# Kernel optimization log

Measured on AMD Instinct MI355X. Metric: run time of the kernel, lower is better.

The kernel has to match this reference:

```python
import jax, jax.numpy as jnp
import numpy as np

N, D = 8192, 256
NEG_BIG = -9e15


def setup_inputs() -> dict:
    key = jax.random.key(0)
    k1, k2, k3 = jax.random.split(key, 3)
    h = jax.random.normal(k1, (N, D), dtype=jnp.float32)
    adj = jax.random.randint(k2, (N, N), 0, 2, dtype=jnp.int32)
    # xavier_uniform for a of shape (2D, 1): bound = sqrt(6/(2D+1))
    bound = np.sqrt(6.0 / (2 * D + 1)).astype(np.float32)
    a = jax.random.uniform(k3, (2 * D, 1), dtype=jnp.float32, minval=-bound, maxval=bound)
    return {"h": h, "adj": adj, "a": a}


def reference(h, adj, a):
    d = h.shape[1]
    h1 = h @ a[:d]            # [N, 1]
    h2 = h @ a[d:]            # [N, 1]
    e = jax.nn.leaky_relu(h1 + h2.T, negative_slope=0.01)  # [N, N]
    attention = jnp.where(adj > 0, e, NEG_BIG)
    attention = jax.nn.softmax(attention, axis=1)
    # dropout skipped: eval mode (training=False)
    return attention @ h      # [N, D]
```

## Files before the change

kernel.cpp:

```cpp
#include <hip/hip_runtime.h>
#include <hip/hip_bf16.h>

#define NTOT 8192
#define DDIM 256
#define ROWS 32
#define JCHUNK (NTOT / 8)
#define NITER (JCHUNK / 32)
#define NWORDS (NTOT / 32)
#define NTSTR 131584

typedef __attribute__((ext_vector_type(8))) short short8;
typedef __attribute__((ext_vector_type(4))) float floatx4;

__global__ __launch_bounds__(256) void gat_scores(const float* __restrict__ h,
                                                  const float* __restrict__ a,
                                                  float* __restrict__ s1,
                                                  float* __restrict__ s2,
                                                  float4* __restrict__ rc,
                                                  float2* __restrict__ etab) {
  int row  = blockIdx.x * 4 + (threadIdx.x >> 6);
  int lane = threadIdx.x & 63;
  const float* hr = h + (size_t)row * DDIM;
  float p1 = 0.f, p2 = 0.f;
#pragma unroll
  for (int k = 0; k < DDIM / 64; ++k) {
    int idx  = lane + 64 * k;
    float hv = hr[idx];
    p1 += hv * a[idx];
    p2 += hv * a[DDIM + idx];
  }
#pragma unroll
  for (int off = 32; off > 0; off >>= 1) {
    p1 += __shfl_down(p1, off, 64);
    p2 += __shfl_down(p2, off, 64);
  }
  if (lane == 0) {
    s1[row] = p1; s2[row] = p2;
    rc[row]   = make_float4(__expf(p1), __expf(0.01f * p1), __expf(-p1), 0.f);
    etab[row] = make_float2(__expf(p2), __expf(0.01f * p2));
  }
}

__global__ __launch_bounds__(256) void gat_pack(const int* __restrict__ adj,
                                                unsigned* __restrict__ bitsT) {
  __shared__ unsigned words[64][65];
  const int t    = threadIdx.x;
  const int lane = t & 63;
  const int w    = t >> 6;
  const int r0   = blockIdx.x * 64;
  const int jb   = blockIdx.y * 2048;

#pragma unroll 2
  for (int rr = 0; rr < 16; ++rr) {
    const int rl = w * 16 + rr;
    const int* ap = adj + (size_t)(r0 + rl) * NTOT + jb + lane * 4;
#pragma unroll
    for (int R = 0; R < 8; ++R) {
      int4 v = *(const int4*)(ap + R * 256);
      unsigned nib = (v.x > 0 ? 1u : 0u) | (v.y > 0 ? 2u : 0u) |
                     (v.z > 0 ? 4u : 0u) | (v.w > 0 ? 8u : 0u);
      unsigned b8  = nib | (__shfl_xor((int)nib, 1, 64) << 4);
      unsigned b16 = b8  | (__shfl_xor((int)b8,  2, 64) << 8);
      unsigned b32 = b16 | (__shfl_xor((int)b16, 4, 64) << 16);
      if ((lane & 7) == 0) words[rl][R * 8 + (lane >> 3)] = b32;
    }
  }
  __syncthreads();

#pragma unroll 4
  for (int kk = 0; kk < 16; ++kk) {
    const int jwl = w * 16 + kk;
    bitsT[(size_t)(jb / 32 + jwl) * NTOT + r0 + lane] = words[lane][jwl];
  }
}

__global__ __launch_bounds__(256) void gat_hpack(const float* __restrict__ h,
                                                 ushort* __restrict__ hTf) {
  __shared__ float tile[64][257];
  const int t    = threadIdx.x;
  const int lane = t & 63;
  const int w    = t >> 6;
  const int quad = lane >> 4;
  const int c    = lane & 15;
  const int i0   = blockIdx.x * 64;

#pragma unroll
  for (int it = 0; it < 16; ++it) {
    int r = it * 4 + w;
    float4 v = *(const float4*)(h + (size_t)(i0 + r) * DDIM + lane * 4);
    tile[r][lane * 4 + 0] = v.x; tile[r][lane * 4 + 1] = v.y;
    tile[r][lane * 4 + 2] = v.z; tile[r][lane * 4 + 3] = v.w;
  }
  __syncthreads();

#pragma unroll
  for (int k = 0; k < 4; ++k) {
    const int n = 4 * k + w;
#pragma unroll
    for (int jbl = 0; jbl < 2; ++jbl) {
      short8 vv;
#pragma unroll
      for (int i = 0; i < 8; ++i) {
        float f = tile[jbl * 32 + quad * 8 + i][n * 16 + c];
        __hip_bfloat16 b = __float2bfloat16(f);
        vv[i] = *(short*)&b;
      }
      *(short8*)(hTf + ((size_t)(n * 257 + i0 / 32 + jbl) * 64 + lane) * 8) = vv;
    }
  }
}

__global__ __launch_bounds__(512, 2) void gat_attn(const ushort* __restrict__ hTf,
                                                   const unsigned* __restrict__ bitsT,
                                                   const float4* __restrict__ rc,
                                                   const float2* __restrict__ etab,
                                                   float* __restrict__ out) {
  __shared__ union {
    float lred[8][32];
    float slab[4][ROWS * 128];
  } sh;

  const int t    = threadIdx.x;
  const int lane = t & 63;
  const int w    = t >> 6;
  const int quad = lane >> 4;
  const int c    = lane & 15;
  const int r0   = blockIdx.x * ROWS;

  const float4 rc0 = rc[r0 + c];
  const float4 rc1 = rc[r0 + 16 + c];
  const float E10 = rc0.x, E20 = rc0.y, T0 = rc0.z;
  const float E11 = rc1.x, E21 = rc1.y, T1 = rc1.z;

  const unsigned* btp = bitsT + (size_t)(w * 32) * NTOT;
  const float*    etb = (const float*)(etab + (size_t)w * JCHUNK + quad * 8);
  const ushort*   hfp = hTf + ((size_t)(w * 32) * 64 + lane) * 8;

  floatx4 acc[2][16];
#pragma unroll
  for (int rt = 0; rt < 2; ++rt)
#pragma unroll
    for (int nt = 0; nt < 16; ++nt) acc[rt][nt] = (floatx4){0.f, 0.f, 0.f, 0.f};

  float lp0 = 0.f, lp1 = 0.f;
  short8 bA[8], bB[8];

  #define LDH(dst, jt, half)                                                   \
    _Pragma("unroll")                                                          \
    for (int q = 0; q < 8; ++q)                                                \
      dst[q] = *(const short8*)(hfp + (size_t)(jt) * 512 +                     \
                                (size_t)((half) * 8 + q) * NTSTR);

  LDH(bA, 0, 0)
  unsigned W0 = btp[r0 + c];
  unsigned W1 = btp[r0 + 16 + c];
  float4 ea = ((const float4*)etb)[0];
  float4 eb = ((const float4*)etb)[1];
  float4 ec = ((const float4*)etb)[2];
  float4 ed = ((const float4*)etb)[3];

  for (int jt = 0; jt < NITER; ++jt) {
    LDH(bB, jt, 1)

    const unsigned bm0 = (W0 >> (quad * 8)) & 0xff;
    const unsigned bm1 = (W1 >> (quad * 8)) & 0xff;
    float tp[16] = {ea.x, ea.y, ea.z, ea.w, eb.x, eb.y, eb.z, eb.w,
                    ec.x, ec.y, ec.z, ec.w, ed.x, ed.y, ed.z, ed.w};
    short8 pa0, pa1;
#pragma unroll
    for (int i = 0; i < 8; ++i) {
      const float t1 = tp[2 * i], t2 = tp[2 * i + 1];
      const float m0 = (float)((bm0 >> i) & 1u);
      const float m1 = (float)((bm1 >> i) & 1u);
      float p0 = ((t1 > T0) ? E10 * t1 : E20 * t2) * m0;
      float p1 = ((t1 > T1) ? E11 * t1 : E21 * t2) * m1;
      lp0 += p0; lp1 += p1;
      __hip_bfloat16 b0 = __float2bfloat16(p0);
      __hip_bfloat16 b1 = __float2bfloat16(p1);
      pa0[i] = *(short*)&b0;
      pa1[i] = *(short*)&b1;
    }

    if (jt + 1 < NITER) {
      W0 = btp[(size_t)(jt + 1) * NTOT + r0 + c];
      W1 = btp[(size_t)(jt + 1) * NTOT + r0 + 16 + c];
      const float* en = etb + (jt + 1) * 64;
      ea = ((const float4*)en)[0];
      eb = ((const float4*)en)[1];
      ec = ((const float4*)en)[2];
      ed = ((const float4*)en)[3];
    }

#pragma unroll
    for (int q = 0; q < 8; ++q) {
      acc[0][q] = __builtin_amdgcn_mfma_f32_16x16x32_bf16(pa0, bA[q], acc[0][q], 0, 0, 0);
      acc[1][q] = __builtin_amdgcn_mfma_f32_16x16x32_bf16(pa1, bA[q], acc[1][q], 0, 0, 0);
    }
    if (jt + 1 < NITER) { LDH(bA, jt + 1, 0) }

#pragma unroll
    for (int q = 0; q < 8; ++q) {
      acc[0][8 + q] = __builtin_amdgcn_mfma_f32_16x16x32_bf16(pa0, bB[q], acc[0][8 + q], 0, 0, 0);
      acc[1][8 + q] = __builtin_amdgcn_mfma_f32_16x16x32_bf16(pa1, bB[q], acc[1][8 + q], 0, 0, 0);
    }
  }
  #undef LDH

  lp0 += __shfl_xor(lp0, 16, 64); lp0 += __shfl_xor(lp0, 32, 64);
  lp1 += __shfl_xor(lp1, 16, 64); lp1 += __shfl_xor(lp1, 32, 64);
  if (quad == 0) { sh.lred[w][c] = lp0; sh.lred[w][16 + c] = lp1; }
  __syncthreads();

  float linv[2][4];
  if (w == 0) {
#pragma unroll
    for (int rt = 0; rt < 2; ++rt)
#pragma unroll
      for (int reg = 0; reg < 4; ++reg) {
        int lrow = rt * 16 + quad * 4 + reg;
        float s = 0.f;
#pragma unroll
        for (int wi = 0; wi < 8; ++wi) s += sh.lred[wi][lrow];
        linv[rt][reg] = 1.f / s;
      }
  }
  __syncthreads();

#pragma unroll
  for (int hd = 0; hd < 2; ++hd) {
    if (w >= 4) {
#pragma unroll
      for (int rt = 0; rt < 2; ++rt)
#pragma unroll
        for (int i = 0; i < 8; ++i)
#pragma unroll
          for (int reg = 0; reg < 4; ++reg)
            sh.slab[w - 4][(rt * 16 + quad * 4 + reg) * 128 + i * 16 + c] =
                acc[rt][i + 8 * hd][reg];
    }
    __syncthreads();
    if (w < 4) {
#pragma unroll
      for (int rt = 0; rt < 2; ++rt)
#pragma unroll
        for (int i = 0; i < 8; ++i)
#pragma unroll
          for (int reg = 0; reg < 4; ++reg)
            acc[rt][i + 8 * hd][reg] +=
                sh.slab[w][(rt * 16 + quad * 4 + reg) * 128 + i * 16 + c];
    }
    __syncthreads();
    if (w == 2 || w == 3) {
#pragma unroll
      for (int rt = 0; rt < 2; ++rt)
#pragma unroll
        for (int i = 0; i < 8; ++i)
#pragma unroll
          for (int reg = 0; reg < 4; ++reg)
            sh.slab[w - 2][(rt * 16 + quad * 4 + reg) * 128 + i * 16 + c] =
                acc[rt][i + 8 * hd][reg];
    }
    __syncthreads();
    if (w < 2) {
#pragma unroll
      for (int rt = 0; rt < 2; ++rt)
#pragma unroll
        for (int i = 0; i < 8; ++i)
#pragma unroll
          for (int reg = 0; reg < 4; ++reg)
            acc[rt][i + 8 * hd][reg] +=
                sh.slab[w][(rt * 16 + quad * 4 + reg) * 128 + i * 16 + c];
    }
    __syncthreads();
    if (w == 1) {
#pragma unroll
      for (int rt = 0; rt < 2; ++rt)
#pragma unroll
        for (int i = 0; i < 8; ++i)
#pragma unroll
          for (int reg = 0; reg < 4; ++reg)
            sh.slab[0][(rt * 16 + quad * 4 + reg) * 128 + i * 16 + c] =
                acc[rt][i + 8 * hd][reg];
    }
    __syncthreads();
    if (w == 0) {
#pragma unroll
      for (int rt = 0; rt < 2; ++rt)
#pragma unroll
        for (int i = 0; i < 8; ++i)
#pragma unroll
          for (int reg = 0; reg < 4; ++reg) {
            float v = acc[rt][i + 8 * hd][reg] +
                      sh.slab[0][(rt * 16 + quad * 4 + reg) * 128 + i * 16 + c];
            out[(size_t)(r0 + rt * 16 + quad * 4 + reg) * DDIM +
                hd * 128 + i * 16 + c] = v * linv[rt][reg];
          }
    }
    __syncthreads();
  }
}

extern "C" void kernel_launch(void* const* d_in, const int* in_sizes, int n_in,
                              void* d_out, int out_size, void* d_ws, size_t ws_size,
                              hipStream_t stream) {
  const float* h   = (const float*)d_in[0];
  const int*   adj = (const int*)d_in[1];
  const float* a   = (const float*)d_in[2];
  float* out = (float*)d_out;

  float*    s1    = (float*)d_ws;
  float*    s2    = s1 + NTOT;
  float4*   rc    = (float4*)(s2 + NTOT);
  float2*   etab  = (float2*)(rc + NTOT);
  unsigned* bitsT = (unsigned*)(etab + NTOT);
  ushort*   hTf   = (ushort*)(bitsT + (size_t)NWORDS * NTOT);

  gat_scores<<<NTOT / 4, 256, 0, stream>>>(h, a, s1, s2, rc, etab);
  gat_pack<<<dim3(NTOT / 64, 4), 256, 0, stream>>>(adj, bitsT);
  gat_hpack<<<NTOT / 64, 256, 0, stream>>>(h, hTf);
  gat_attn<<<NTOT / ROWS, 512, 0, stream>>>(hTf, bitsT, rc, etab, out);
}
```

Before: 453.7 us.

## Fuse adjacency packing into attention kernel, reading int32 adj directly

Drops the separate bit-packing kernel and has the attention kernel load the int32 adjacency rows directly, eight consecutive ints per lane per iteration, for its two rows. This removes one kernel launch and the write and re-read of the packed bit matrix. In exchange the attention kernel now streams the full 256 MB int32 adjacency itself, with row-strided per-lane loads, and uses more vector registers. The leaky-relu branch is also rewritten as fmaxf of the two exponential terms, which drops the threshold value.

```diff
diff --git a/kernel.cpp b/kernel.cpp
--- a/kernel.cpp
+++ b/kernel.cpp
@@ -6,16 +6,14 @@
 #define ROWS 32
 #define JCHUNK (NTOT / 8)
 #define NITER (JCHUNK / 32)
-#define NWORDS (NTOT / 32)
 #define NTSTR 131584
 
 typedef __attribute__((ext_vector_type(8))) short short8;
 typedef __attribute__((ext_vector_type(4))) float floatx4;
+typedef __attribute__((ext_vector_type(4))) int intx4;
 
 __global__ __launch_bounds__(256) void gat_scores(const float* __restrict__ h,
                                                   const float* __restrict__ a,
-                                                  float* __restrict__ s1,
-                                                  float* __restrict__ s2,
                                                   float4* __restrict__ rc,
                                                   float2* __restrict__ etab) {
   int row  = blockIdx.x * 4 + (threadIdx.x >> 6);
@@ -35,42 +33,8 @@
     p2 += __shfl_down(p2, off, 64);
   }
   if (lane == 0) {
-    s1[row] = p1; s2[row] = p2;
-    rc[row]   = make_float4(__expf(p1), __expf(0.01f * p1), __expf(-p1), 0.f);
+    rc[row]   = make_float4(__expf(p1), __expf(0.01f * p1), 0.f, 0.f);
     etab[row] = make_float2(__expf(p2), __expf(0.01f * p2));
-  }
-}
-
-__global__ __launch_bounds__(256) void gat_pack(const int* __restrict__ adj,
-                                                unsigned* __restrict__ bitsT) {
-  __shared__ unsigned words[64][65];
-  const int t    = threadIdx.x;
-  const int lane = t & 63;
-  const int w    = t >> 6;
-  const int r0   = blockIdx.x * 64;
-  const int jb   = blockIdx.y * 2048;
-
-#pragma unroll 2
-  for (int rr = 0; rr < 16; ++rr) {
-    const int rl = w * 16 + rr;
-    const int* ap = adj + (size_t)(r0 + rl) * NTOT + jb + lane * 4;
-#pragma unroll
-    for (int R = 0; R < 8; ++R) {
-      int4 v = *(const int4*)(ap + R * 256);
-      unsigned nib = (v.x > 0 ? 1u : 0u) | (v.y > 0 ? 2u : 0u) |
-                     (v.z > 0 ? 4u : 0u) | (v.w > 0 ? 8u : 0u);
-      unsigned b8  = nib | (__shfl_xor((int)nib, 1, 64) << 4);
-      unsigned b16 = b8  | (__shfl_xor((int)b8,  2, 64) << 8);
-      unsigned b32 = b16 | (__shfl_xor((int)b16, 4, 64) << 16);
-      if ((lane & 7) == 0) words[rl][R * 8 + (lane >> 3)] = b32;
-    }
-  }
-  __syncthreads();
-
-#pragma unroll 4
-  for (int kk = 0; kk < 16; ++kk) {
-    const int jwl = w * 16 + kk;
-    bitsT[(size_t)(jb / 32 + jwl) * NTOT + r0 + lane] = words[lane][jwl];
   }
 }
 
@@ -111,7 +75,7 @@
 }
 
 __global__ __launch_bounds__(512, 2) void gat_attn(const ushort* __restrict__ hTf,
-                                                   const unsigned* __restrict__ bitsT,
+                                                   const int* __restrict__ adj,
                                                    const float4* __restrict__ rc,
                                                    const float2* __restrict__ etab,
                                                    float* __restrict__ out) {
@@ -129,10 +93,11 @@
 
   const float4 rc0 = rc[r0 + c];
   const float4 rc1 = rc[r0 + 16 + c];
-  const float E10 = rc0.x, E20 = rc0.y, T0 = rc0.z;
-  const float E11 = rc1.x, E21 = rc1.y, T1 = rc1.z;
-
-  const unsigned* btp = bitsT + (size_t)(w * 32) * NTOT;
+  const float E10 = rc0.x, E20 = rc0.y;
+  const float E11 = rc1.x, E21 = rc1.y;
+
+  const int* ap0 = adj + (size_t)(r0 + c) * NTOT + (size_t)w * JCHUNK + quad * 8;
+  const int* ap1 = ap0 + (size_t)16 * NTOT;
   const float*    etb = (const float*)(etab + (size_t)w * JCHUNK + quad * 8);
   const ushort*   hfp = hTf + ((size_t)(w * 32) * 64 + lane) * 8;
 
@@ -152,8 +117,10 @@
                                 (size_t)((half) * 8 + q) * NTSTR);
 
   LDH(bA, 0, 0)
-  unsigned W0 = btp[r0 + c];
-  unsigned W1 = btp[r0 + 16 + c];
+  intx4 A0a = *(const intx4*)ap0;
+  intx4 A0b = *(const intx4*)(ap0 + 4);
+  intx4 A1a = *(const intx4*)ap1;
+  intx4 A1b = *(const intx4*)(ap1 + 4);
   float4 ea = ((const float4*)etb)[0];
   float4 eb = ((const float4*)etb)[1];
   float4 ec = ((const float4*)etb)[2];
@@ -162,18 +129,16 @@
   for (int jt = 0; jt < NITER; ++jt) {
     LDH(bB, jt, 1)
 
-    const unsigned bm0 = (W0 >> (quad * 8)) & 0xff;
-    const unsigned bm1 = (W1 >> (quad * 8)) & 0xff;
+    const int am0[8] = {A0a[0], A0a[1], A0a[2], A0a[3], A0b[0], A0b[1], A0b[2], A0b[3]};
+    const int am1[8] = {A1a[0], A1a[1], A1a[2], A1a[3], A1b[0], A1b[1], A1b[2], A1b[3]};
     float tp[16] = {ea.x, ea.y, ea.z, ea.w, eb.x, eb.y, eb.z, eb.w,
                     ec.x, ec.y, ec.z, ec.w, ed.x, ed.y, ed.z, ed.w};
     short8 pa0, pa1;
 #pragma unroll
     for (int i = 0; i < 8; ++i) {
       const float t1 = tp[2 * i], t2 = tp[2 * i + 1];
-      const float m0 = (float)((bm0 >> i) & 1u);
-      const float m1 = (float)((bm1 >> i) & 1u);
-      float p0 = ((t1 > T0) ? E10 * t1 : E20 * t2) * m0;
-      float p1 = ((t1 > T1) ? E11 * t1 : E21 * t2) * m1;
+      float p0 = (am0[i] > 0) ? fmaxf(E10 * t1, E20 * t2) : 0.f;
+      float p1 = (am1[i] > 0) ? fmaxf(E11 * t1, E21 * t2) : 0.f;
       lp0 += p0; lp1 += p1;
       __hip_bfloat16 b0 = __float2bfloat16(p0);
       __hip_bfloat16 b1 = __float2bfloat16(p1);
@@ -182,8 +147,12 @@
     }
 
     if (jt + 1 < NITER) {
-      W0 = btp[(size_t)(jt + 1) * NTOT + r0 + c];
-      W1 = btp[(size_t)(jt + 1) * NTOT + r0 + 16 + c];
+      const int* n0 = ap0 + (size_t)(jt + 1) * 32;
+      A0a = *(const intx4*)n0;
+      A0b = *(const intx4*)(n0 + 4);
+      const int* n1 = ap1 + (size_t)(jt + 1) * 32;
+      A1a = *(const intx4*)n1;
+      A1b = *(const intx4*)(n1 + 4);
       const float* en = etb + (jt + 1) * 64;
       ea = ((const float4*)en)[0];
       eb = ((const float4*)en)[1];
@@ -308,15 +277,11 @@
   const float* a   = (const float*)d_in[2];
   float* out = (float*)d_out;
 
-  float*    s1    = (float*)d_ws;
-  float*    s2    = s1 + NTOT;
-  float4*   rc    = (float4*)(s2 + NTOT);
+  float4*   rc    = (float4*)d_ws;
   float2*   etab  = (float2*)(rc + NTOT);
-  unsigned* bitsT = (unsigned*)(etab + NTOT);
-  ushort*   hTf   = (ushort*)(bitsT + (size_t)NWORDS * NTOT);
-
-  gat_scores<<<NTOT / 4, 256, 0, stream>>>(h, a, s1, s2, rc, etab);
-  gat_pack<<<dim3(NTOT / 64, 4), 256, 0, stream>>>(adj, bitsT);
+  ushort*   hTf   = (ushort*)(etab + NTOT);
+
+  gat_scores<<<NTOT / 4, 256, 0, stream>>>(h, a, rc, etab);
   gat_hpack<<<NTOT / 64, 256, 0, stream>>>(h, hTf);
-  gat_attn<<<NTOT / ROWS, 512, 0, stream>>>(hTf, bitsT, rc, etab, out);
-}
+  gat_attn<<<NTOT / ROWS, 512, 0, stream>>>(hTf, adj, rc, etab, out);
+}
```

Result: faster. 442.9 us (-2.4%).
